# Kernel tuning notes

Measured on AMD Instinct MI355X. Metric: run time of the kernel, lower is better.

Reference implementation:

```python
import jax, jax.numpy as jnp
import numpy as np

EPS = 1e-12

def _normalize(x, axis=-1):
    # matches torch F.normalize(dim=-1) with default eps=1e-12
    n = jnp.linalg.norm(x, axis=axis, keepdims=True)
    return x / jnp.maximum(n, EPS)

def setup_inputs() -> dict:
    key = jax.random.key(0)
    k1, k2, k3 = jax.random.split(key, 3)
    B, D, C = 262144, 256, 128
    dirs = jax.random.normal(k1, (B, D), dtype=jnp.float32)
    v_class = _normalize(jax.random.normal(k2, (C, D), dtype=jnp.float32))
    labels = jax.random.randint(k3, (B,), 0, C, dtype=jnp.int32)
    return {"dirs": dirs, "v_class": v_class, "labels": labels, "step": 100}

def reference(dirs, v_class, labels, step):
    n_classes, _ = v_class.shape
    ema_alpha = 0.02
    proto_weight = 0.1

    dirs_n = _normalize(dirs)                      # (B, D)

    # ---- EMA update (no-grad in original; segment-mean per class) ----
    d = jax.lax.stop_gradient(dirs_n)
    sums = jax.ops.segment_sum(d, labels, num_segments=n_classes)      # (C, D)
    counts = jax.ops.segment_sum(jnp.ones((d.shape[0],), d.dtype), labels,
                                 num_segments=n_classes)               # (C,)
    batch_mean = sums / jnp.maximum(counts, 1.0)[:, None]
    batch_mean = _normalize(batch_mean)
    alpha = min(ema_alpha, step / (step + 50))
    updated = _normalize((1.0 - alpha) * v_class + alpha * batch_mean)
    new_v = jnp.where((counts > 0)[:, None], updated, v_class)         # (C, D)
    new_v = jax.lax.stop_gradient(new_v)  # buffer: no grad flows through it

    # ---- prototype alignment loss ----
    protos = new_v[labels]                          # (B, D) gather
    cos_sim = jnp.sum(dirs_n * protos, axis=-1)     # (B,)
    l_proto = jnp.mean(1.0 - cos_sim)
    return proto_weight * l_proto, new_v
```

## Files before the change

### kernel.cpp

```cpp
#include <hip/hip_runtime.h>


#define PF_D 256
#define PF_C 128
#define PF_SCALE 524288.0f
#define PF_INV_SCALE (1.0f / 524288.0f)

__device__ __forceinline__ float pf_wave_sum(float v) {
  #pragma unroll
  for (int m = 1; m < 64; m <<= 1) v += __shfl_xor(v, m, 64);
  return v;
}

__global__ void pf_zero(int* __restrict__ ws, int n) {
  int i = blockIdx.x * blockDim.x + threadIdx.x;
  if (i < n) ws[i] = 0;
}

__global__ __launch_bounds__(1024) void pf_accum(
    const float* __restrict__ dirs, const int* __restrict__ labels,
    int* __restrict__ gsum, int* __restrict__ gcnt, int B) {
  __shared__ int lacc[PF_C * PF_D];
  __shared__ int lnum[PF_C];
  const int tid = threadIdx.x;
  for (int i = tid; i < PF_C * PF_D; i += 1024) lacc[i] = 0;
  if (tid < PF_C) lnum[tid] = 0;
  __syncthreads();

  const int lane = tid & 63;
  const int wave = tid >> 6;
  const int rows_per_block = (B + (int)gridDim.x - 1) / (int)gridDim.x;
  const int row_lo = blockIdx.x * rows_per_block;
  const int row_hi = min(B, row_lo + rows_per_block);
  const int rows_per_wave = (rows_per_block + 15) >> 4;
  const int w_lo = row_lo + wave * rows_per_wave;
  const int w_hi = min(row_hi, w_lo + rows_per_wave);

  int r = w_lo;
  for (; r + 4 <= w_hi; r += 4) {
    float4 v0 = ((const float4*)(dirs + (size_t)(r + 0) * PF_D))[lane];
    float4 v1 = ((const float4*)(dirs + (size_t)(r + 1) * PF_D))[lane];
    float4 v2 = ((const float4*)(dirs + (size_t)(r + 2) * PF_D))[lane];
    float4 v3 = ((const float4*)(dirs + (size_t)(r + 3) * PF_D))[lane];
    int c0 = labels[r + 0], c1 = labels[r + 1];
    int c2 = labels[r + 2], c3 = labels[r + 3];
    float s0 = v0.x * v0.x + v0.y * v0.y + v0.z * v0.z + v0.w * v0.w;
    float s1 = v1.x * v1.x + v1.y * v1.y + v1.z * v1.z + v1.w * v1.w;
    float s2 = v2.x * v2.x + v2.y * v2.y + v2.z * v2.z + v2.w * v2.w;
    float s3 = v3.x * v3.x + v3.y * v3.y + v3.z * v3.z + v3.w * v3.w;
    #pragma unroll
    for (int m = 1; m < 64; m <<= 1) {
      s0 += __shfl_xor(s0, m, 64);
      s1 += __shfl_xor(s1, m, 64);
      s2 += __shfl_xor(s2, m, 64);
      s3 += __shfl_xor(s3, m, 64);
    }
    float k0 = PF_SCALE / fmaxf(sqrtf(s0), 1e-12f);
    float k1 = PF_SCALE / fmaxf(sqrtf(s1), 1e-12f);
    float k2 = PF_SCALE / fmaxf(sqrtf(s2), 1e-12f);
    float k3 = PF_SCALE / fmaxf(sqrtf(s3), 1e-12f);
    int* p0 = lacc + c0 * PF_D;
    int* p1 = lacc + c1 * PF_D;
    int* p2 = lacc + c2 * PF_D;
    int* p3 = lacc + c3 * PF_D;
    atomicAdd(p0 + lane,       __float2int_rn(v0.x * k0));
    atomicAdd(p1 + lane,       __float2int_rn(v1.x * k1));
    atomicAdd(p2 + lane,       __float2int_rn(v2.x * k2));
    atomicAdd(p3 + lane,       __float2int_rn(v3.x * k3));
    atomicAdd(p0 + 64 + lane,  __float2int_rn(v0.y * k0));
    atomicAdd(p1 + 64 + lane,  __float2int_rn(v1.y * k1));
    atomicAdd(p2 + 64 + lane,  __float2int_rn(v2.y * k2));
    atomicAdd(p3 + 64 + lane,  __float2int_rn(v3.y * k3));
    atomicAdd(p0 + 128 + lane, __float2int_rn(v0.z * k0));
    atomicAdd(p1 + 128 + lane, __float2int_rn(v1.z * k1));
    atomicAdd(p2 + 128 + lane, __float2int_rn(v2.z * k2));
    atomicAdd(p3 + 128 + lane, __float2int_rn(v3.z * k3));
    atomicAdd(p0 + 192 + lane, __float2int_rn(v0.w * k0));
    atomicAdd(p1 + 192 + lane, __float2int_rn(v1.w * k1));
    atomicAdd(p2 + 192 + lane, __float2int_rn(v2.w * k2));
    atomicAdd(p3 + 192 + lane, __float2int_rn(v3.w * k3));
    if (lane < 4) {
      int cc = (lane == 0) ? c0 : (lane == 1) ? c1 : (lane == 2) ? c2 : c3;
      atomicAdd(&lnum[cc], 1);
    }
  }
  for (; r < w_hi; r++) {
    float4 v = ((const float4*)(dirs + (size_t)r * PF_D))[lane];
    float sq = pf_wave_sum(v.x * v.x + v.y * v.y + v.z * v.z + v.w * v.w);
    float k = PF_SCALE / fmaxf(sqrtf(sq), 1e-12f);
    int cls = labels[r];
    int* p = lacc + cls * PF_D;
    atomicAdd(p + lane,       __float2int_rn(v.x * k));
    atomicAdd(p + 64  + lane, __float2int_rn(v.y * k));
    atomicAdd(p + 128 + lane, __float2int_rn(v.z * k));
    atomicAdd(p + 192 + lane, __float2int_rn(v.w * k));
    if (lane == 0) atomicAdd(&lnum[cls], 1);
  }
  __syncthreads();

  for (int i = tid; i < PF_C * PF_D; i += 1024) {
    int s = lacc[i];
    if (s != 0) atomicAdd(&gsum[i], s);
  }
  if (tid < PF_C) {
    int s = lnum[tid];
    if (s != 0) atomicAdd(&gcnt[tid], s);
  }
}

__global__ __launch_bounds__(64) void pf_cls(
    const int* __restrict__ gsum, const int* __restrict__ gcnt,
    const float* __restrict__ v_class, const int* __restrict__ step_ptr,
    float* __restrict__ out, float* __restrict__ dots) {
  const int c = blockIdx.x;
  const int lane = threadIdx.x;
  const float stepf = (float)step_ptr[0];
  const float alpha = fminf(0.02f, stepf / (stepf + 50.f));

  const int cnt = gcnt[c];
  const float denom = fmaxf((float)cnt, 1.f);
  float s[4], vc[4], bm[4];
  float nb = 0.f;
  #pragma unroll
  for (int j = 0; j < 4; j++) {
    int e = lane + 64 * j;
    s[j]  = (float)gsum[c * PF_D + ((e & 3) << 6) + (e >> 2)] * PF_INV_SCALE;
    vc[j] = v_class[c * PF_D + e];
    bm[j] = s[j] / denom;
    nb += bm[j] * bm[j];
  }
  nb = pf_wave_sum(nb);
  const float rb = 1.f / fmaxf(sqrtf(nb), 1e-12f);
  float u[4];
  float nu = 0.f;
  #pragma unroll
  for (int j = 0; j < 4; j++) {
    u[j] = (1.f - alpha) * vc[j] + alpha * (bm[j] * rb);
    nu += u[j] * u[j];
  }
  nu = pf_wave_sum(nu);
  const float ru = 1.f / fmaxf(sqrtf(nu), 1e-12f);
  float dacc = 0.f;
  #pragma unroll
  for (int j = 0; j < 4; j++) {
    int e = lane + 64 * j;
    float nv = (cnt > 0) ? u[j] * ru : vc[j];
    out[1 + c * PF_D + e] = nv;
    dacc += s[j] * nv;
  }
  dacc = pf_wave_sum(dacc);
  if (lane == 0) dots[c] = dacc;
}

__global__ __launch_bounds__(128) void pf_loss(
    const float* __restrict__ dots, float* __restrict__ out, int B) {
  const int tid = threadIdx.x;
  float v = dots[tid];
  v = pf_wave_sum(v);
  __shared__ float part[2];
  if ((tid & 63) == 0) part[tid >> 6] = v;
  __syncthreads();
  if (tid == 0) out[0] = 0.1f * (1.f - (part[0] + part[1]) / (float)B);
}

extern "C" void kernel_launch(void* const* d_in, const int* in_sizes, int n_in,
                              void* d_out, int out_size, void* d_ws, size_t ws_size,
                              hipStream_t stream) {
  const float* dirs    = (const float*)d_in[0];
  const float* v_class = (const float*)d_in[1];
  const int*   labels  = (const int*)d_in[2];
  const int*   step    = (const int*)d_in[3];
  const int B = in_sizes[2];

  int*   gsum = (int*)d_ws;
  int*   gcnt = gsum + PF_C * PF_D;
  float* dots = (float*)(gcnt + PF_C);
  const int nzero = PF_C * PF_D + PF_C;

  pf_zero<<<(nzero + 255) / 256, 256, 0, stream>>>(gsum, nzero);
  pf_accum<<<256, 1024, 0, stream>>>(dirs, labels, gsum, gcnt, B);
  pf_cls<<<PF_C, 64, 0, stream>>>(gsum, gcnt, v_class, step,
                                  (float*)d_out, dots);
  pf_loss<<<1, 128, 0, stream>>>(dots, (float*)d_out, B);
}
```

Measured before the change: 389.4 us.

## Replace global atomic reduction with per-block partials and fused final loss

Each accumulation block now writes its full shared-memory histogram to a private partial buffer with vector stores, replacing the per-element global atomics and the zeroing kernel. The class kernel reduces the 256 partials per class with 256 threads. The separate loss kernel is folded in through a ticket semaphore, with the last class block writing the loss. This removes two launches and global atomic contention, but adds about 32 MB of partial-buffer traffic and relies on static device globals that the last block resets.

```diff
diff --git a/kernel.cpp b/kernel.cpp
--- a/kernel.cpp
+++ b/kernel.cpp
@@ -3,23 +3,29 @@
 
 #define PF_D 256
 #define PF_C 128
+#define PF_NB 256
 #define PF_SCALE 524288.0f
 #define PF_INV_SCALE (1.0f / 524288.0f)
 
+__device__ __align__(16) int g_part[PF_NB][PF_C * PF_D];
+__device__ int g_pcnt[PF_NB][PF_C];
+__device__ float g_loss;
+__device__ int g_sem;
+
 __device__ __forceinline__ float pf_wave_sum(float v) {
   #pragma unroll
   for (int m = 1; m < 64; m <<= 1) v += __shfl_xor(v, m, 64);
   return v;
 }
 
-__global__ void pf_zero(int* __restrict__ ws, int n) {
-  int i = blockIdx.x * blockDim.x + threadIdx.x;
-  if (i < n) ws[i] = 0;
+__device__ __forceinline__ int pf_wave_isum(int v) {
+  #pragma unroll
+  for (int m = 1; m < 64; m <<= 1) v += __shfl_xor(v, m, 64);
+  return v;
 }
 
 __global__ __launch_bounds__(1024) void pf_accum(
-    const float* __restrict__ dirs, const int* __restrict__ labels,
-    int* __restrict__ gsum, int* __restrict__ gcnt, int B) {
+    const float* __restrict__ dirs, const int* __restrict__ labels, int B) {
   __shared__ int lacc[PF_C * PF_D];
   __shared__ int lnum[PF_C];
   const int tid = threadIdx.x;
@@ -98,33 +104,56 @@
   }
   __syncthreads();
 
-  for (int i = tid; i < PF_C * PF_D; i += 1024) {
-    int s = lacc[i];
-    if (s != 0) atomicAdd(&gsum[i], s);
-  }
-  if (tid < PF_C) {
-    int s = lnum[tid];
-    if (s != 0) atomicAdd(&gcnt[tid], s);
-  }
-}
-
-__global__ __launch_bounds__(64) void pf_cls(
-    const int* __restrict__ gsum, const int* __restrict__ gcnt,
+  int4* gp4 = (int4*)g_part[blockIdx.x];
+  const int4* l4 = (const int4*)lacc;
+  for (int i = tid; i < (PF_C * PF_D) / 4; i += 1024) gp4[i] = l4[i];
+  if (tid < PF_C) g_pcnt[blockIdx.x][tid] = lnum[tid];
+}
+
+__global__ __launch_bounds__(256) void pf_cls(
     const float* __restrict__ v_class, const int* __restrict__ step_ptr,
-    float* __restrict__ out, float* __restrict__ dots) {
+    float* __restrict__ out, int B) {
   const int c = blockIdx.x;
-  const int lane = threadIdx.x;
+  const int tid = threadIdx.x;
+  const int lane = tid & 63;
+  const int wave = tid >> 6;
+
+  __shared__ int acc[PF_D];
+  __shared__ int scnt;
+  if (tid < PF_D) acc[tid] = 0;
+  if (tid == 0) scnt = 0;
+  __syncthreads();
+
+  int mc = g_pcnt[tid][c];
+  mc = pf_wave_isum(mc);
+  if (lane == 0) atomicAdd(&scnt, mc);
+
+  int ax = 0, ay = 0, az = 0, aw = 0;
+  #pragma unroll 8
+  for (int k = 0; k < 64; ++k) {
+    const int b = wave * 64 + k;
+    const int4 t = ((const int4*)(g_part[b] + c * PF_D))[lane];
+    ax += t.x; ay += t.y; az += t.z; aw += t.w;
+  }
+  atomicAdd(&acc[4 * lane + 0], ax);
+  atomicAdd(&acc[4 * lane + 1], ay);
+  atomicAdd(&acc[4 * lane + 2], az);
+  atomicAdd(&acc[4 * lane + 3], aw);
+  __syncthreads();
+
+  if (wave != 0) return;
+
   const float stepf = (float)step_ptr[0];
   const float alpha = fminf(0.02f, stepf / (stepf + 50.f));
-
-  const int cnt = gcnt[c];
+  const int cnt = scnt;
   const float denom = fmaxf((float)cnt, 1.f);
+
   float s[4], vc[4], bm[4];
   float nb = 0.f;
   #pragma unroll
   for (int j = 0; j < 4; j++) {
     int e = lane + 64 * j;
-    s[j]  = (float)gsum[c * PF_D + ((e & 3) << 6) + (e >> 2)] * PF_INV_SCALE;
+    s[j]  = (float)acc[((e & 3) << 6) + (e >> 2)] * PF_INV_SCALE;
     vc[j] = v_class[c * PF_D + e];
     bm[j] = s[j] / denom;
     nb += bm[j] * bm[j];
@@ -149,18 +178,18 @@
     dacc += s[j] * nv;
   }
   dacc = pf_wave_sum(dacc);
-  if (lane == 0) dots[c] = dacc;
-}
-
-__global__ __launch_bounds__(128) void pf_loss(
-    const float* __restrict__ dots, float* __restrict__ out, int B) {
-  const int tid = threadIdx.x;
-  float v = dots[tid];
-  v = pf_wave_sum(v);
-  __shared__ float part[2];
-  if ((tid & 63) == 0) part[tid >> 6] = v;
-  __syncthreads();
-  if (tid == 0) out[0] = 0.1f * (1.f - (part[0] + part[1]) / (float)B);
+
+  if (lane == 0) {
+    atomicAdd(&g_loss, dacc);
+    __threadfence();
+    const int ticket = atomicAdd(&g_sem, 1);
+    if (ticket == PF_C - 1) {
+      __threadfence();
+      const float total = atomicExch(&g_loss, 0.f);
+      out[0] = 0.1f * (1.f - total / (float)B);
+      atomicExch(&g_sem, 0);
+    }
+  }
 }
 
 extern "C" void kernel_launch(void* const* d_in, const int* in_sizes, int n_in,
@@ -172,14 +201,8 @@
   const int*   step    = (const int*)d_in[3];
   const int B = in_sizes[2];
 
-  int*   gsum = (int*)d_ws;
-  int*   gcnt = gsum + PF_C * PF_D;
-  float* dots = (float*)(gcnt + PF_C);
-  const int nzero = PF_C * PF_D + PF_C;
-
-  pf_zero<<<(nzero + 255) / 256, 256, 0, stream>>>(gsum, nzero);
-  pf_accum<<<256, 1024, 0, stream>>>(dirs, labels, gsum, gcnt, B);
-  pf_cls<<<PF_C, 64, 0, stream>>>(gsum, gcnt, v_class, step,
-                                  (float*)d_out, dots);
-  pf_loss<<<1, 128, 0, stream>>>(dots, (float*)d_out, B);
-}
+  (void)d_ws; (void)ws_size;
+
+  pf_accum<<<PF_NB, 1024, 0, stream>>>(dirs, labels, B);
+  pf_cls<<<PF_C, 256, 0, stream>>>(v_class, step, (float*)d_out, B);
+}
```

After: 388.5 us. Within noise of the previous version (-0.2%).
